# Kernel tuning notes

Hardware: AMD Instinct MI355X
Metric: run time of the kernel (lower is better)

## Reference

```python
import jax, jax.numpy as jnp
import numpy as np

B, S, D_IN, D_OUT = 4, 2048, 4096, 4096


def setup_inputs() -> dict:
    key = jax.random.key(0)
    k_x, k_w, k_s, k_b = jax.random.split(key, 4)
    x = jax.random.normal(k_x, (B, S, D_IN), dtype=jnp.float32)
    # simulated int8 compressed weight, values in [-128, 127]
    weight_int8 = jax.random.randint(k_w, (D_OUT, D_IN), 0, 255, dtype=jnp.int32) - 128
    # per-output-row dequant scale (positive)
    scale = jax.random.uniform(k_s, (D_OUT,), dtype=jnp.float32) * 0.01 + 1e-4
    bias = jax.random.normal(k_b, (D_OUT,), dtype=jnp.float32)
    return {"x": x, "weight_int8": weight_int8, "scale": scale, "bias": bias}


def reference(x, weight_int8, scale, bias):
    # dequantize: int8 -> fp, per-row scale, reshape to (out, in)
    weight_fp = weight_int8.astype(x.dtype) * scale[:, None]  # [D_OUT, D_IN]
    # F.linear: x @ W^T + b
    out = jnp.einsum("bsd,od->bso", x, weight_fp) + bias
    return out
```

## Files before the change

kernel.cpp:

```cpp
#include <hip/hip_runtime.h>


#define BM 256
#define BN 256
#define BKB 128

constexpr int Mdim = 8192;
constexpr int Ndim = 4096;
constexpr int Kdim = 4096;
constexpr int KT = Kdim / BKB;

typedef __attribute__((ext_vector_type(4)))  int   int32x4;
typedef __attribute__((ext_vector_type(16))) int   int32x16;
typedef __attribute__((ext_vector_type(8)))  short short8;
typedef __attribute__((ext_vector_type(4)))  float f32x4;
typedef unsigned short ushort_t;

__device__ __forceinline__ unsigned short f2bf(float f) {
    union { float f; unsigned u; } v; v.f = f;
    unsigned r = v.u + 0x7FFFu + ((v.u >> 16) & 1u);
    return (unsigned short)(r >> 16);
}

__device__ __forceinline__ void gload_lds16(const void* g, void* l) {
    __builtin_amdgcn_global_load_lds(
        (const __attribute__((address_space(1))) void*)g,
        (__attribute__((address_space(3))) void*)l, 16, 0, 0);
}

#define BARRIER() __builtin_amdgcn_s_barrier()
#define WAITV0()  asm volatile("s_waitcnt vmcnt(0)" ::: "memory")
#define WAITV4()  asm volatile("s_waitcnt vmcnt(4)" ::: "memory")

#define CLUSTER(MBASE) do {                                                  \
    __builtin_amdgcn_s_setprio(1);                                           \
    _Pragma("unroll") for (int mt = 0; mt < 2; ++mt)                         \
    _Pragma("unroll") for (int nt = 0; nt < 2; ++nt)                         \
    _Pragma("unroll") for (int ks = 0; ks < 4; ++ks)                         \
        acc[(MBASE)+mt][nt] = __builtin_amdgcn_mfma_i32_32x32x32_i8(         \
            af[mt][ks], bf[nt][ks], acc[(MBASE)+mt][nt], 0, 0, 0);           \
    __builtin_amdgcn_s_setprio(0);                                           \
} while (0)


__global__ __launch_bounds__(256)
void quant_x_rowwise(const float* __restrict__ x, char* __restrict__ xq,
                     float* __restrict__ sx) {
    const int row = blockIdx.x;
    const float4* xr = reinterpret_cast<const float4*>(x + (size_t)row * Kdim);
    const int tid = threadIdx.x;
    float4 v[4];
    float am = 0.f;
    #pragma unroll
    for (int j = 0; j < 4; ++j) {
        v[j] = xr[tid + 256 * j];
        am = fmaxf(am, fmaxf(fmaxf(fabsf(v[j].x), fabsf(v[j].y)),
                             fmaxf(fabsf(v[j].z), fabsf(v[j].w))));
    }
    #pragma unroll
    for (int off = 32; off; off >>= 1)
        am = fmaxf(am, __shfl_xor(am, off, 64));
    __shared__ float red[4];
    if ((tid & 63) == 0) red[tid >> 6] = am;
    __syncthreads();
    am = fmaxf(fmaxf(red[0], red[1]), fmaxf(red[2], red[3]));
    am = fmaxf(am, 1e-30f);
    if (tid == 0) sx[row] = am / 127.f;
    const float inv = 127.f / am;
    int* outw = reinterpret_cast<int*>(xq + (size_t)row * Kdim);
    #pragma unroll
    for (int j = 0; j < 4; ++j) {
        const int q0 = (int)rintf(v[j].x * inv) & 255;
        const int q1 = (int)rintf(v[j].y * inv) & 255;
        const int q2 = (int)rintf(v[j].z * inv) & 255;
        const int q3 = (int)rintf(v[j].w * inv) & 255;
        outw[tid + 256 * j] = q0 | (q1 << 8) | (q2 << 16) | (q3 << 24);
    }
}

__global__ __launch_bounds__(256)
void pack_w_int8(const int* __restrict__ w, char* __restrict__ wq, int n4) {
    int idx = blockIdx.x * blockDim.x + threadIdx.x;
    const int stride = gridDim.x * blockDim.x;
    int* out = reinterpret_cast<int*>(wq);
    for (int i = idx; i < n4; i += stride) {
        const int4 a = reinterpret_cast<const int4*>(w)[i];
        out[i] = (a.x & 255) | ((a.y & 255) << 8) |
                 ((a.z & 255) << 16) | ((a.w & 255) << 24);
    }
}


__global__ __launch_bounds__(512, 2)
void gemm_i8_flat(const char* __restrict__ A,
                  const char* __restrict__ B,
                  const float* __restrict__ scale,
                  const float* __restrict__ bias,
                  const float* __restrict__ sx,
                  float* __restrict__ Out)
{
    __shared__ __align__(16) char smem[2][4][16384];

    const int tid = threadIdx.x;
    int bid = blockIdx.x;
    bid = (bid & 7) * 64 + (bid >> 3);
    const int tn = bid & 15;
    const int tm = bid >> 4;
    const int brow = tm * BM;
    const int bcol = tn * BN;

    const int lane = tid & 63;
    const int w    = tid >> 6;
    const int wr   = w >> 2;
    const int wc   = w & 3;
    const int r32  = lane & 31;
    const int h    = lane >> 5;
    const size_t K1 = (size_t)Kdim;

    const int swzb = ((lane & 7) ^ (lane >> 3) ^ (w & 3)) << 4;
    const char* aStageSrc = A + (size_t)(brow + w * 8 + (lane >> 3)) * K1 + swzb;
    const char* bStageSrc = B + (size_t)(bcol + w * 8 + (lane >> 3)) * K1 + swzb;

    auto stageA = [&](int bufb, int hh, int tt) {
        const char* s = aStageSrc + (size_t)(hh * 128) * K1 + (size_t)tt * BKB;
        char* d = &smem[bufb][hh][w * 1024];
        gload_lds16(s, d);
        gload_lds16(s + 64 * K1, d + 8192);
    };
    auto stageB = [&](int bufb, int hh, int tt) {
        const char* s = bStageSrc + (size_t)(hh * 128) * K1 + (size_t)tt * BKB;
        char* d = &smem[bufb][2 + hh][w * 1024];
        gload_lds16(s, d);
        gload_lds16(s + 64 * K1, d + 8192);
    };

    const char* aBase[2] = { &smem[0][wr][0] + r32 * 128,
                             &smem[1][wr][0] + r32 * 128 };
    const char* bBase[2] = { &smem[0][2 + (wc >> 1)][0] + ((wc & 1) * 64 + r32) * 128,
                             &smem[1][2 + (wc >> 1)][0] + ((wc & 1) * 64 + r32) * 128 };
    const int frx = ((r32 & 7) ^ (r32 >> 3)) << 4;
    int colb[4];
    #pragma unroll
    for (int ks = 0; ks < 4; ++ks) colb[ks] = (ks * 32 + h * 16) ^ frx;

    int32x16 acc[4][2] = {};
    int32x4 af[2][4], bf[2][4];

    auto ldA = [&](const char* base, int MH) {
        #pragma unroll
        for (int mt = 0; mt < 2; ++mt) {
            const char* p = base + ((MH) * 2 + mt) * 4096;
            #pragma unroll
            for (int ks = 0; ks < 4; ++ks)
                af[mt][ks] = *reinterpret_cast<const int32x4*>(p + colb[ks]);
        }
    };
    auto ldB = [&](const char* base) {
        #pragma unroll
        for (int nt = 0; nt < 2; ++nt) {
            const char* p = base + nt * 4096;
            #pragma unroll
            for (int ks = 0; ks < 4; ++ks)
                bf[nt][ks] = *reinterpret_cast<const int32x4*>(p + colb[ks]);
        }
    };

    stageA(0, 0, 0); stageA(0, 1, 0);
    stageB(0, 0, 0); stageB(0, 1, 0);
    stageB(1, 0, 1); stageB(1, 1, 1);
    WAITV4();
    BARRIER();

    for (int i = 0; i < KT / 2 - 1; ++i) {
        const int t = 2 * i;

        ldB(bBase[0]); ldA(aBase[0], 0);
        BARRIER();
        CLUSTER(0);
        ldA(aBase[0], 1);
        stageA(1, 0, t + 1); stageA(1, 1, t + 1);
        stageB(0, 0, t + 2); stageB(0, 1, t + 2);
        CLUSTER(2);
        WAITV4();
        BARRIER();

        ldB(bBase[1]); ldA(aBase[1], 0);
        BARRIER();
        CLUSTER(0);
        ldA(aBase[1], 1);
        stageA(0, 0, t + 2); stageA(0, 1, t + 2);
        stageB(1, 0, t + 3); stageB(1, 1, t + 3);
        CLUSTER(2);
        WAITV4();
        BARRIER();
    }

    {
        ldB(bBase[0]); ldA(aBase[0], 0);
        BARRIER();
        CLUSTER(0);
        ldA(aBase[0], 1);
        stageA(1, 0, KT - 1); stageA(1, 1, KT - 1);
        CLUSTER(2);
        WAITV0();
        BARRIER();
    }
    {
        ldB(bBase[1]); ldA(aBase[1], 0);
        BARRIER();
        CLUSTER(0);
        ldA(aBase[1], 1);
        CLUSTER(2);
    }

    #pragma unroll
    for (int nt = 0; nt < 2; ++nt) {
        const int col = bcol + wc * 64 + nt * 32 + r32;
        const float sc = scale[col];
        const float bi = bias[col];
        #pragma unroll
        for (int mt = 0; mt < 4; ++mt) {
            const int rb = brow + wr * 128 + mt * 32 + 4 * h;
            #pragma unroll
            for (int q = 0; q < 4; ++q) {
                const int r4 = rb + 8 * q;
                #pragma unroll
                for (int r = 0; r < 4; ++r) {
                    const float sxr = sx[r4 + r];
                    Out[(size_t)(r4 + r) * Ndim + col] =
                        (float)acc[mt][nt][q * 4 + r] * (sc * sxr) + bi;
                }
            }
        }
    }
}


__device__ __forceinline__ int swz_fb(int row, int colbyte) {
    return row * 128 + (colbyte ^ ((row & 7) << 4));
}

__global__ __launch_bounds__(256)
void compressed_linear_fb(const float* __restrict__ X,
                          const int*   __restrict__ W,
                          const float* __restrict__ scale,
                          const float* __restrict__ bias,
                          float* __restrict__ Out)
{
    __shared__ __align__(16) ushort_t lA[128 * 64];
    __shared__ __align__(16) ushort_t lB[128 * 64];
    const int tid = threadIdx.x;
    const int bid = blockIdx.x;
    const int tn = bid & 31, tm = bid >> 5;
    const int brow = tm * 128, bcol = tn * 128;
    const int r0 = tid >> 3, c0 = tid & 7;
    float4 aPre[4][2]; int4 bPre[4][2];
    const int lane = tid & 63, w = tid >> 6;
    const int wr = w >> 1, wc = w & 1, fr = lane & 15, fq = lane >> 4;
    f32x4 acc[4][4] = {};

    auto loadTiles = [&](int t) {
        const int k0 = t * 64;
        #pragma unroll
        for (int i = 0; i < 4; i++) {
            const int row = r0 + 32 * i;
            const float4* pa = reinterpret_cast<const float4*>(X + (size_t)(brow + row) * Kdim + k0 + c0 * 8);
            aPre[i][0] = pa[0]; aPre[i][1] = pa[1];
            const int4* pb = reinterpret_cast<const int4*>(W + (size_t)(bcol + row) * Kdim + k0 + c0 * 8);
            bPre[i][0] = pb[0]; bPre[i][1] = pb[1];
        }
    };
    auto writeLDS = [&]() {
        #pragma unroll
        for (int i = 0; i < 4; i++) {
            const int row = r0 + 32 * i;
            const int off = swz_fb(row, c0 * 16);
            short8 va, vb;
            va[0] = (short)f2bf(aPre[i][0].x); va[1] = (short)f2bf(aPre[i][0].y);
            va[2] = (short)f2bf(aPre[i][0].z); va[3] = (short)f2bf(aPre[i][0].w);
            va[4] = (short)f2bf(aPre[i][1].x); va[5] = (short)f2bf(aPre[i][1].y);
            va[6] = (short)f2bf(aPre[i][1].z); va[7] = (short)f2bf(aPre[i][1].w);
            vb[0] = (short)f2bf((float)bPre[i][0].x); vb[1] = (short)f2bf((float)bPre[i][0].y);
            vb[2] = (short)f2bf((float)bPre[i][0].z); vb[3] = (short)f2bf((float)bPre[i][0].w);
            vb[4] = (short)f2bf((float)bPre[i][1].x); vb[5] = (short)f2bf((float)bPre[i][1].y);
            vb[6] = (short)f2bf((float)bPre[i][1].z); vb[7] = (short)f2bf((float)bPre[i][1].w);
            *reinterpret_cast<short8*>(reinterpret_cast<char*>(lA) + off) = va;
            *reinterpret_cast<short8*>(reinterpret_cast<char*>(lB) + off) = vb;
        }
    };

    loadTiles(0);
    for (int t = 0; t < Kdim / 64; t++) {
        writeLDS();
        __syncthreads();
        if (t + 1 < Kdim / 64) loadTiles(t + 1);
        #pragma unroll
        for (int kk = 0; kk < 2; kk++) {
            short8 afv[4], bfv[4];
            const int cb = kk * 64 + fq * 16;
            #pragma unroll
            for (int m = 0; m < 4; m++) {
                const int row = wr * 64 + m * 16 + fr;
                afv[m] = *reinterpret_cast<const short8*>(reinterpret_cast<const char*>(lA) + swz_fb(row, cb));
            }
            #pragma unroll
            for (int n = 0; n < 4; n++) {
                const int row = wc * 64 + n * 16 + fr;
                bfv[n] = *reinterpret_cast<const short8*>(reinterpret_cast<const char*>(lB) + swz_fb(row, cb));
            }
            #pragma unroll
            for (int m = 0; m < 4; m++)
                #pragma unroll
                for (int n = 0; n < 4; n++)
                    acc[m][n] = __builtin_amdgcn_mfma_f32_16x16x32_bf16(afv[m], bfv[n], acc[m][n], 0, 0, 0);
        }
        __syncthreads();
    }
    #pragma unroll
    for (int n = 0; n < 4; n++) {
        const int col = bcol + wc * 64 + n * 16 + fr;
        const float sc = scale[col];
        const float bi = bias[col];
        #pragma unroll
        for (int m = 0; m < 4; m++) {
            const int rbase = brow + wr * 64 + m * 16 + fq * 4;
            #pragma unroll
            for (int j = 0; j < 4; j++)
                Out[(size_t)(rbase + j) * Ndim + col] = acc[m][n][j] * sc + bi;
        }
    }
}


extern "C" void kernel_launch(void* const* d_in, const int* in_sizes, int n_in,
                              void* d_out, int out_size, void* d_ws, size_t ws_size,
                              hipStream_t stream) {
    const float* x     = (const float*)d_in[0];
    const int*   w8    = (const int*)d_in[1];
    const float* scale = (const float*)d_in[2];
    const float* bias  = (const float*)d_in[3];
    float* out = (float*)d_out;

    const size_t xq_bytes = (size_t)Mdim * Kdim;
    const size_t wq_bytes = (size_t)Ndim * Kdim;
    const size_t sx_bytes = (size_t)Mdim * sizeof(float);

    if (ws_size >= xq_bytes + wq_bytes + sx_bytes) {
        char*  xq = (char*)d_ws;
        char*  wq = (char*)d_ws + xq_bytes;
        float* sx = (float*)((char*)d_ws + xq_bytes + wq_bytes);
        quant_x_rowwise<<<Mdim, 256, 0, stream>>>(x, xq, sx);
        pack_w_int8<<<2048, 256, 0, stream>>>(w8, wq, (Ndim * Kdim) / 4);
        dim3 grid((Mdim / BM) * (Ndim / BN));
        gemm_i8_flat<<<grid, dim3(512), 0, stream>>>(xq, wq, scale, bias, sx, out);
    } else {
        dim3 grid((Mdim / 128) * (Ndim / 128));
        compressed_linear_fb<<<grid, dim3(256), 0, stream>>>(x, w8, scale, bias, out);
    }
}
```

Baseline: 194.5 us.

## Replace split half-tile staging with simple full-tile double-buffered GEMM pipeline

Drops the interleaved half-tile schedule, where A and B halves were staged at offsets with vmcnt(4) waits and several barriers per step. The int8 GEMM now uses a plain double buffer: each k-step prefetches the whole next A/B tile, loads all fragments from LDS, runs all MFMAs, then waits on vmcnt(0) and hits one barrier. This cuts barriers and is simpler, but it holds more fragment registers (af01, af23 and bf all live at once). It also serialises the full LDS fragment load ahead of the MFMAs, so LDS reads overlap less with compute.

```diff
diff --git a/kernel.cpp b/kernel.cpp
--- a/kernel.cpp
+++ b/kernel.cpp
@@ -30,17 +30,6 @@
 
 #define BARRIER() __builtin_amdgcn_s_barrier()
 #define WAITV0()  asm volatile("s_waitcnt vmcnt(0)" ::: "memory")
-#define WAITV4()  asm volatile("s_waitcnt vmcnt(4)" ::: "memory")
-
-#define CLUSTER(MBASE) do {                                                  \
-    __builtin_amdgcn_s_setprio(1);                                           \
-    _Pragma("unroll") for (int mt = 0; mt < 2; ++mt)                         \
-    _Pragma("unroll") for (int nt = 0; nt < 2; ++nt)                         \
-    _Pragma("unroll") for (int ks = 0; ks < 4; ++ks)                         \
-        acc[(MBASE)+mt][nt] = __builtin_amdgcn_mfma_i32_32x32x32_i8(         \
-            af[mt][ks], bf[nt][ks], acc[(MBASE)+mt][nt], 0, 0, 0);           \
-    __builtin_amdgcn_s_setprio(0);                                           \
-} while (0)
 
 
 __global__ __launch_bounds__(256)
@@ -92,14 +81,14 @@
 
 
 __global__ __launch_bounds__(512, 2)
-void gemm_i8_flat(const char* __restrict__ A,
+void gemm_i8_pipe(const char* __restrict__ A,
                   const char* __restrict__ B,
                   const float* __restrict__ scale,
                   const float* __restrict__ bias,
                   const float* __restrict__ sx,
                   float* __restrict__ Out)
 {
-    __shared__ __align__(16) char smem[2][4][16384];
+    __shared__ __align__(16) char smem[2][2][32768];
 
     const int tid = threadIdx.x;
     int bid = blockIdx.x;
@@ -121,96 +110,91 @@
     const char* aStageSrc = A + (size_t)(brow + w * 8 + (lane >> 3)) * K1 + swzb;
     const char* bStageSrc = B + (size_t)(bcol + w * 8 + (lane >> 3)) * K1 + swzb;
 
-    auto stageA = [&](int bufb, int hh, int tt) {
-        const char* s = aStageSrc + (size_t)(hh * 128) * K1 + (size_t)tt * BKB;
-        char* d = &smem[bufb][hh][w * 1024];
-        gload_lds16(s, d);
-        gload_lds16(s + 64 * K1, d + 8192);
-    };
-    auto stageB = [&](int bufb, int hh, int tt) {
-        const char* s = bStageSrc + (size_t)(hh * 128) * K1 + (size_t)tt * BKB;
-        char* d = &smem[bufb][2 + hh][w * 1024];
-        gload_lds16(s, d);
-        gload_lds16(s + 64 * K1, d + 8192);
-    };
-
-    const char* aBase[2] = { &smem[0][wr][0] + r32 * 128,
-                             &smem[1][wr][0] + r32 * 128 };
-    const char* bBase[2] = { &smem[0][2 + (wc >> 1)][0] + ((wc & 1) * 64 + r32) * 128,
-                             &smem[1][2 + (wc >> 1)][0] + ((wc & 1) * 64 + r32) * 128 };
+    auto stageA = [&](int bufb, int tt) {
+        const char* s = aStageSrc + (size_t)tt * BKB;
+        char* d = &smem[bufb][0][w * 1024];
+        #pragma unroll
+        for (int i = 0; i < 4; ++i)
+            gload_lds16(s + (size_t)(64 * i) * K1, d + i * 8192);
+    };
+    auto stageB = [&](int bufb, int tt) {
+        const char* s = bStageSrc + (size_t)tt * BKB;
+        char* d = &smem[bufb][1][w * 1024];
+        #pragma unroll
+        for (int i = 0; i < 4; ++i)
+            gload_lds16(s + (size_t)(64 * i) * K1, d + i * 8192);
+    };
+
+    const char* aBase[2] = { &smem[0][0][0] + r32 * 128 + wr * 16384,
+                             &smem[1][0][0] + r32 * 128 + wr * 16384 };
+    const char* bBase[2] = { &smem[0][1][0] + (wc * 64 + r32) * 128,
+                             &smem[1][1][0] + (wc * 64 + r32) * 128 };
     const int frx = ((r32 & 7) ^ (r32 >> 3)) << 4;
     int colb[4];
     #pragma unroll
     for (int ks = 0; ks < 4; ++ks) colb[ks] = (ks * 32 + h * 16) ^ frx;
 
     int32x16 acc[4][2] = {};
-    int32x4 af[2][4], bf[2][4];
-
-    auto ldA = [&](const char* base, int MH) {
-        #pragma unroll
-        for (int mt = 0; mt < 2; ++mt) {
-            const char* p = base + ((MH) * 2 + mt) * 4096;
+    int32x4 af01[2][4], af23[2][4], bf[2][4];
+
+    auto ldB = [&](const char* base) {
+        #pragma unroll
+        for (int nt = 0; nt < 2; ++nt)
             #pragma unroll
             for (int ks = 0; ks < 4; ++ks)
-                af[mt][ks] = *reinterpret_cast<const int32x4*>(p + colb[ks]);
-        }
-    };
-    auto ldB = [&](const char* base) {
-        #pragma unroll
-        for (int nt = 0; nt < 2; ++nt) {
-            const char* p = base + nt * 4096;
+                bf[nt][ks] = *reinterpret_cast<const int32x4*>(base + nt * 4096 + colb[ks]);
+    };
+    auto ldA01 = [&](const char* base) {
+        #pragma unroll
+        for (int mt = 0; mt < 2; ++mt)
             #pragma unroll
             for (int ks = 0; ks < 4; ++ks)
-                bf[nt][ks] = *reinterpret_cast<const int32x4*>(p + colb[ks]);
-        }
-    };
-
-    stageA(0, 0, 0); stageA(0, 1, 0);
-    stageB(0, 0, 0); stageB(0, 1, 0);
-    stageB(1, 0, 1); stageB(1, 1, 1);
-    WAITV4();
+                af01[mt][ks] = *reinterpret_cast<const int32x4*>(base + mt * 4096 + colb[ks]);
+    };
+    auto ldA23 = [&](const char* base) {
+        #pragma unroll
+        for (int mt = 0; mt < 2; ++mt)
+            #pragma unroll
+            for (int ks = 0; ks < 4; ++ks)
+                af23[mt][ks] = *reinterpret_cast<const int32x4*>(base + (2 + mt) * 4096 + colb[ks]);
+    };
+
+    stageA(0, 0); stageB(0, 0);
+    WAITV0();
     BARRIER();
 
-    for (int i = 0; i < KT / 2 - 1; ++i) {
-        const int t = 2 * i;
-
-        ldB(bBase[0]); ldA(aBase[0], 0);
-        BARRIER();
-        CLUSTER(0);
-        ldA(aBase[0], 1);
-        stageA(1, 0, t + 1); stageA(1, 1, t + 1);
-        stageB(0, 0, t + 2); stageB(0, 1, t + 2);
-        CLUSTER(2);
-        WAITV4();
-        BARRIER();
-
-        ldB(bBase[1]); ldA(aBase[1], 0);
-        BARRIER();
-        CLUSTER(0);
-        ldA(aBase[1], 1);
-        stageA(0, 0, t + 2); stageA(0, 1, t + 2);
-        stageB(1, 0, t + 3); stageB(1, 1, t + 3);
-        CLUSTER(2);
-        WAITV4();
-        BARRIER();
-    }
-
-    {
-        ldB(bBase[0]); ldA(aBase[0], 0);
-        BARRIER();
-        CLUSTER(0);
-        ldA(aBase[0], 1);
-        stageA(1, 0, KT - 1); stageA(1, 1, KT - 1);
-        CLUSTER(2);
+    for (int t = 0; t < KT; ++t) {
+        const int c = t & 1;
+        if (t + 1 < KT) { stageA(1 - c, t + 1); stageB(1 - c, t + 1); }
+
+        ldB(bBase[c]);
+        ldA01(aBase[c]);
+        ldA23(aBase[c]);
+
+        __builtin_amdgcn_s_setprio(1);
+        #pragma unroll
+        for (int mt = 0; mt < 2; ++mt)
+            #pragma unroll
+            for (int nt = 0; nt < 2; ++nt)
+                #pragma unroll
+                for (int ks = 0; ks < 4; ++ks)
+                    acc[mt][nt] = __builtin_amdgcn_mfma_i32_32x32x32_i8(
+                        af01[mt][ks], bf[nt][ks], acc[mt][nt], 0, 0, 0);
+        __builtin_amdgcn_s_setprio(0);
+
+        __builtin_amdgcn_s_setprio(1);
+        #pragma unroll
+        for (int mt = 0; mt < 2; ++mt)
+            #pragma unroll
+            for (int nt = 0; nt < 2; ++nt)
+                #pragma unroll
+                for (int ks = 0; ks < 4; ++ks)
+                    acc[2 + mt][nt] = __builtin_amdgcn_mfma_i32_32x32x32_i8(
+                        af23[mt][ks], bf[nt][ks], acc[2 + mt][nt], 0, 0, 0);
+        __builtin_amdgcn_s_setprio(0);
+
         WAITV0();
         BARRIER();
-    }
-    {
-        ldB(bBase[1]); ldA(aBase[1], 0);
-        BARRIER();
-        CLUSTER(0);
-        ldA(aBase[1], 1);
-        CLUSTER(2);
     }
 
     #pragma unroll
@@ -352,7 +336,7 @@
         quant_x_rowwise<<<Mdim, 256, 0, stream>>>(x, xq, sx);
         pack_w_int8<<<2048, 256, 0, stream>>>(w8, wq, (Ndim * Kdim) / 4);
         dim3 grid((Mdim / BM) * (Ndim / BN));
-        gemm_i8_flat<<<grid, dim3(512), 0, stream>>>(xq, wq, scale, bias, sx, out);
+        gemm_i8_pipe<<<grid, dim3(512), 0, stream>>>(xq, wq, scale, bias, sx, out);
     } else {
         dim3 grid((Mdim / 128) * (Ndim / 128));
         compressed_linear_fb<<<grid, dim3(256), 0, stream>>>(x, w8, scale, bias, out);
```

Result: slower. 274.5 us (+41.1%).

## Spread global-to-LDS staging across four MFMA clusters with ping-pong A fragments

Applied to the files above, without the earlier changes.

Restructures the int8 GEMM main loop so each K-tile is split into four per-m-tile MFMA clusters. A fragments are double-buffered in registers (afA/afB), and the global_load_lds stages are interleaved one per cluster instead of issued in bursts. The aim is to hide LDS reads and global traffic behind MFMA work more evenly and to lower A-fragment register pressure. It adds more barriers per iteration, and the epilogue now hoists the sx loads per m-tile.

```diff
diff --git a/kernel.cpp b/kernel.cpp
--- a/kernel.cpp
+++ b/kernel.cpp
@@ -32,13 +32,12 @@
 #define WAITV0()  asm volatile("s_waitcnt vmcnt(0)" ::: "memory")
 #define WAITV4()  asm volatile("s_waitcnt vmcnt(4)" ::: "memory")
 
-#define CLUSTER(MBASE) do {                                                  \
+#define CL(AF, MT) do {                                                      \
     __builtin_amdgcn_s_setprio(1);                                           \
-    _Pragma("unroll") for (int mt = 0; mt < 2; ++mt)                         \
+    _Pragma("unroll") for (int ks = 0; ks < 4; ++ks)                         \
     _Pragma("unroll") for (int nt = 0; nt < 2; ++nt)                         \
-    _Pragma("unroll") for (int ks = 0; ks < 4; ++ks)                         \
-        acc[(MBASE)+mt][nt] = __builtin_amdgcn_mfma_i32_32x32x32_i8(         \
-            af[mt][ks], bf[nt][ks], acc[(MBASE)+mt][nt], 0, 0, 0);           \
+        acc[MT][nt] = __builtin_amdgcn_mfma_i32_32x32x32_i8(                 \
+            AF[ks], bf[nt][ks], acc[MT][nt], 0, 0, 0);                       \
     __builtin_amdgcn_s_setprio(0);                                           \
 } while (0)
 
@@ -92,12 +91,12 @@
 
 
 __global__ __launch_bounds__(512, 2)
-void gemm_i8_flat(const char* __restrict__ A,
-                  const char* __restrict__ B,
-                  const float* __restrict__ scale,
-                  const float* __restrict__ bias,
-                  const float* __restrict__ sx,
-                  float* __restrict__ Out)
+void gemm_i8_spread(const char* __restrict__ A,
+                    const char* __restrict__ B,
+                    const float* __restrict__ scale,
+                    const float* __restrict__ bias,
+                    const float* __restrict__ sx,
+                    float* __restrict__ Out)
 {
     __shared__ __align__(16) char smem[2][4][16384];
 
@@ -134,101 +133,131 @@
         gload_lds16(s + 64 * K1, d + 8192);
     };
 
-    const char* aBase[2] = { &smem[0][wr][0] + r32 * 128,
-                             &smem[1][wr][0] + r32 * 128 };
-    const char* bBase[2] = { &smem[0][2 + (wc >> 1)][0] + ((wc & 1) * 64 + r32) * 128,
-                             &smem[1][2 + (wc >> 1)][0] + ((wc & 1) * 64 + r32) * 128 };
+    const char* aB0 = &smem[0][wr][0] + r32 * 128;
+    const char* aB1 = &smem[1][wr][0] + r32 * 128;
+    const char* bB0 = &smem[0][2 + (wc >> 1)][0] + ((wc & 1) * 64 + r32) * 128;
+    const char* bB1 = &smem[1][2 + (wc >> 1)][0] + ((wc & 1) * 64 + r32) * 128;
     const int frx = ((r32 & 7) ^ (r32 >> 3)) << 4;
     int colb[4];
     #pragma unroll
     for (int ks = 0; ks < 4; ++ks) colb[ks] = (ks * 32 + h * 16) ^ frx;
 
     int32x16 acc[4][2] = {};
-    int32x4 af[2][4], bf[2][4];
-
-    auto ldA = [&](const char* base, int MH) {
-        #pragma unroll
-        for (int mt = 0; mt < 2; ++mt) {
-            const char* p = base + ((MH) * 2 + mt) * 4096;
+    int32x4 afA[4], afB[4], bf[2][4];
+
+    auto ldAf = [&](int32x4* dst, const char* base, int mt) {
+        #pragma unroll
+        for (int ks = 0; ks < 4; ++ks)
+            dst[ks] = *reinterpret_cast<const int32x4*>(base + mt * 4096 + colb[ks]);
+    };
+    auto ldBf = [&](const char* base) {
+        #pragma unroll
+        for (int nt = 0; nt < 2; ++nt)
             #pragma unroll
             for (int ks = 0; ks < 4; ++ks)
-                af[mt][ks] = *reinterpret_cast<const int32x4*>(p + colb[ks]);
-        }
-    };
-    auto ldB = [&](const char* base) {
-        #pragma unroll
-        for (int nt = 0; nt < 2; ++nt) {
-            const char* p = base + nt * 4096;
-            #pragma unroll
-            for (int ks = 0; ks < 4; ++ks)
-                bf[nt][ks] = *reinterpret_cast<const int32x4*>(p + colb[ks]);
-        }
-    };
-
-    stageA(0, 0, 0); stageA(0, 1, 0);
-    stageB(0, 0, 0); stageB(0, 1, 0);
+                bf[nt][ks] = *reinterpret_cast<const int32x4*>(base + nt * 4096 + colb[ks]);
+    };
+
+    stageB(0, 0, 0); stageB(0, 1, 0); stageA(0, 0, 0); stageA(0, 1, 0);
     stageB(1, 0, 1); stageB(1, 1, 1);
     WAITV4();
     BARRIER();
+    ldAf(afA, aB0, 0);
+    ldBf(bB0);
 
     for (int i = 0; i < KT / 2 - 1; ++i) {
-        const int t = 2 * i;
-
-        ldB(bBase[0]); ldA(aBase[0], 0);
-        BARRIER();
-        CLUSTER(0);
-        ldA(aBase[0], 1);
-        stageA(1, 0, t + 1); stageA(1, 1, t + 1);
-        stageB(0, 0, t + 2); stageB(0, 1, t + 2);
-        CLUSTER(2);
+        const int te = 2 * i;
+        BARRIER();
+        stageA(1, 0, te + 1);
+        CL(afA, 0);
+        ldAf(afB, aB0, 1);
+        BARRIER();
+        stageA(1, 1, te + 1);
+        stageB(0, 0, te + 2);
+        CL(afB, 1);
+        ldAf(afA, aB0, 2);
+        BARRIER();
+        stageB(0, 1, te + 2);
+        CL(afA, 2);
+        ldAf(afB, aB0, 3);
         WAITV4();
         BARRIER();
-
-        ldB(bBase[1]); ldA(aBase[1], 0);
-        BARRIER();
-        CLUSTER(0);
-        ldA(aBase[1], 1);
-        stageA(0, 0, t + 2); stageA(0, 1, t + 2);
-        stageB(1, 0, t + 3); stageB(1, 1, t + 3);
-        CLUSTER(2);
+        CL(afB, 3);
+        ldAf(afA, aB1, 0);
+        ldBf(bB1);
+        BARRIER();
+        stageA(0, 0, te + 2);
+        CL(afA, 0);
+        ldAf(afB, aB1, 1);
+        BARRIER();
+        stageA(0, 1, te + 2);
+        stageB(1, 0, te + 3);
+        CL(afB, 1);
+        ldAf(afA, aB1, 2);
+        BARRIER();
+        stageB(1, 1, te + 3);
+        CL(afA, 2);
+        ldAf(afB, aB1, 3);
         WAITV4();
         BARRIER();
+        CL(afB, 3);
+        ldAf(afA, aB0, 0);
+        ldBf(bB0);
     }
 
     {
-        ldB(bBase[0]); ldA(aBase[0], 0);
-        BARRIER();
-        CLUSTER(0);
-        ldA(aBase[0], 1);
-        stageA(1, 0, KT - 1); stageA(1, 1, KT - 1);
-        CLUSTER(2);
+        BARRIER();
+        stageA(1, 0, KT - 1);
+        CL(afA, 0);
+        ldAf(afB, aB0, 1);
+        BARRIER();
+        stageA(1, 1, KT - 1);
+        CL(afB, 1);
+        ldAf(afA, aB0, 2);
+        BARRIER();
+        CL(afA, 2);
+        ldAf(afB, aB0, 3);
         WAITV0();
         BARRIER();
+        CL(afB, 3);
+        ldAf(afA, aB1, 0);
+        ldBf(bB1);
     }
     {
-        ldB(bBase[1]); ldA(aBase[1], 0);
-        BARRIER();
-        CLUSTER(0);
-        ldA(aBase[1], 1);
-        CLUSTER(2);
-    }
-
-    #pragma unroll
-    for (int nt = 0; nt < 2; ++nt) {
-        const int col = bcol + wc * 64 + nt * 32 + r32;
-        const float sc = scale[col];
-        const float bi = bias[col];
-        #pragma unroll
-        for (int mt = 0; mt < 4; ++mt) {
-            const int rb = brow + wr * 128 + mt * 32 + 4 * h;
+        BARRIER();
+        CL(afA, 0);
+        ldAf(afB, aB1, 1);
+        BARRIER();
+        CL(afB, 1);
+        ldAf(afA, aB1, 2);
+        BARRIER();
+        CL(afA, 2);
+        ldAf(afB, aB1, 3);
+        BARRIER();
+        CL(afB, 3);
+    }
+
+    #pragma unroll
+    for (int mt = 0; mt < 4; ++mt) {
+        const int rb = brow + wr * 128 + mt * 32 + 4 * h;
+        float sxr[4][4];
+        #pragma unroll
+        for (int q = 0; q < 4; ++q)
+            #pragma unroll
+            for (int r = 0; r < 4; ++r)
+                sxr[q][r] = sx[rb + 8 * q + r];
+        #pragma unroll
+        for (int nt = 0; nt < 2; ++nt) {
+            const int col = bcol + wc * 64 + nt * 32 + r32;
+            const float sc = scale[col];
+            const float bi = bias[col];
             #pragma unroll
             for (int q = 0; q < 4; ++q) {
                 const int r4 = rb + 8 * q;
                 #pragma unroll
                 for (int r = 0; r < 4; ++r) {
-                    const float sxr = sx[r4 + r];
                     Out[(size_t)(r4 + r) * Ndim + col] =
-                        (float)acc[mt][nt][q * 4 + r] * (sc * sxr) + bi;
+                        (float)acc[mt][nt][q * 4 + r] * (sc * sxr[q][r]) + bi;
                 }
             }
         }
@@ -352,7 +381,7 @@
         quant_x_rowwise<<<Mdim, 256, 0, stream>>>(x, xq, sx);
         pack_w_int8<<<2048, 256, 0, stream>>>(w8, wq, (Ndim * Kdim) / 4);
         dim3 grid((Mdim / BM) * (Ndim / BN));
-        gemm_i8_flat<<<grid, dim3(512), 0, stream>>>(xq, wq, scale, bias, sx, out);
+        gemm_i8_spread<<<grid, dim3(512), 0, stream>>>(xq, wq, scale, bias, sx, out);
     } else {
         dim3 grid((Mdim / 128) * (Ndim / 128));
         compressed_linear_fb<<<grid, dim3(256), 0, stream>>>(x, w8, scale, bias, out);
```

Result: faster. 189.0 us (-2.8%).
